# Kernel optimization log

Measured on AMD Instinct MI355X. Metric: run time of the kernel, lower is better.

Reference implementation:

```python
import jax, jax.numpy as jnp
import numpy as np

B, N, D = 4, 4096, 1024
H, DH = 16, 64  # heads, dim_head; inner_dim = H*DH = 1024
EPS = 1e-6


def setup_inputs() -> dict:
    key = jax.random.key(0)
    ks = jax.random.split(key, 6)
    s = 1.0 / np.sqrt(D)
    return {
        "x": jax.random.normal(ks[0], (B, N, D), dtype=jnp.float32),
        "Wq": jax.random.normal(ks[1], (D, H * DH), dtype=jnp.float32) * s,
        "Wk": jax.random.normal(ks[2], (D, H * DH), dtype=jnp.float32) * s,
        "Wv": jax.random.normal(ks[3], (D, H * DH), dtype=jnp.float32) * s,
        "Wo": jax.random.normal(ks[4], (H * DH, D), dtype=jnp.float32) * s,
        "bo": jnp.zeros((D,), dtype=jnp.float32),
    }


def reference(x, Wq, Wk, Wv, Wo, bo):
    # projections, split heads: b n (h d) -> b h n d
    def split_heads(t):
        b, n, _ = t.shape
        return t.reshape(b, n, H, DH).transpose(0, 2, 1, 3)

    q = split_heads(x @ Wq)
    k = split_heads(x @ Wk)  # context = x (self-attention)
    v = split_heads(x @ Wv)

    # elu feature map: elu(x) + 1
    q = jax.nn.elu(q) + 1.0
    k = jax.nn.elu(k) + 1.0

    # normalizer z[b,h,n,1] = q . sum_n k  + eps
    k_sum = k.sum(axis=2)                                  # b h d
    z = jnp.einsum('bhnd,bhd->bhn', q, k_sum)[..., None] + EPS

    # kv outer-product reduction: O(N d^2)
    kv = jnp.einsum('bhnd,bhne->bhde', k, v)               # b h d e
    out = jnp.einsum('bhnd,bhde->bhne', q, kv) / z         # b h n e

    # merge heads: b h n d -> b n (h d)
    out = out.transpose(0, 2, 1, 3).reshape(x.shape[0], x.shape[1], H * DH)
    return out @ Wo + bo
```

## Files before the change

### kernel.cpp

```cpp
#include <hip/hip_runtime.h>
#include <hip/hip_bf16.h>


#define DEV_INLINE __device__ __forceinline__

typedef short bf16x8 __attribute__((ext_vector_type(8)));
typedef float f32x4  __attribute__((ext_vector_type(4)));

static constexpr int Bb = 4, Nn = 4096, Dd = 1024, Hh = 16, DHd = 64;
static constexpr int Mrows = Bb * Nn;

DEV_INLINE float bf2f(short s) {
  unsigned u = ((unsigned)(unsigned short)s) << 16;
  float f; __builtin_memcpy(&f, &u, 4); return f;
}
DEV_INLINE short f2bf(float f) {
  unsigned u; __builtin_memcpy(&u, &f, 4);
  unsigned r = (u + 0x7fffu + ((u >> 16) & 1u)) >> 16;
  return (short)r;
}

DEV_INLINE void gload16(const void* g, void* l) {
  typedef __attribute__((address_space(1))) const void gv_t;
  typedef __attribute__((address_space(3))) void lv_t;
  __builtin_amdgcn_global_load_lds((gv_t*)g, (lv_t*)l, 16, 0, 0);
}

DEV_INLINE int lds_off(int r_, int c_) {
  return r_ * 128 + ((((c_ >> 3) ^ (r_ & 7)) << 3) | (c_ & 7));
}


__global__ void convert_x_kernel(const float* __restrict__ x, short* __restrict__ xb) {
  int i = blockIdx.x * 256 + threadIdx.x;
  float4 v = ((const float4*)x)[i];
  short4 o;
  o.x = f2bf(v.x); o.y = f2bf(v.y); o.z = f2bf(v.z); o.w = f2bf(v.w);
  ((short4*)xb)[i] = o;
}

__global__ void transposeW_kernel(const float* __restrict__ W, short* __restrict__ Wt) {
  __shared__ float tile[64][69];
  int t = threadIdx.x;
  int r = t >> 2, c4 = (t & 3) << 4;
  const float* src = W + (blockIdx.y * 64 + r) * 1024 + blockIdx.x * 64 + c4;
  for (int j = 0; j < 4; ++j) {
    float4 v = ((const float4*)src)[j];
    tile[r][c4 + 4 * j + 0] = v.x;
    tile[r][c4 + 4 * j + 1] = v.y;
    tile[r][c4 + 4 * j + 2] = v.z;
    tile[r][c4 + 4 * j + 3] = v.w;
  }
  __syncthreads();
  __attribute__((aligned(16))) short tmp[16];
  for (int j = 0; j < 16; ++j) tmp[j] = f2bf(tile[c4 + j][r]);
  short* dst = Wt + (blockIdx.x * 64 + r) * 1024 + blockIdx.y * 64 + c4;
  ((int4*)dst)[0] = ((int4*)tmp)[0];
  ((int4*)dst)[1] = ((int4*)tmp)[1];
}

template <int MODE>
__global__ __launch_bounds__(256, 2) void gemm128_kernel(
    const short* __restrict__ A, const short* __restrict__ Bt,
    short* __restrict__ q, short* __restrict__ kT, short* __restrict__ vT,
    float* __restrict__ out, const float* __restrict__ bias, int nTilesN) {
  __shared__ __align__(16) short sm[128 * 128];
  short* smA = sm;
  short* smB = sm + 8192;
  const int K = 1024;
  int bid0 = blockIdx.x;
  int xcd = bid0 & 7, local = bid0 >> 3;
  int chunk = local >> 6, rem = local & 63;
  int ncc = nTilesN >> 3;
  int cm = chunk / ncc, cn = chunk % ncc;
  int tm = xcd * 16 + cm * 8 + (rem >> 3);
  int tn = cn * 8 + (rem & 7);

  int t = threadIdx.x, w = t >> 6, lane = t & 63;
  int rl = lane & 15, kg = lane >> 4;
  int wr = w >> 1, wc = w & 1;
  const short* Abase = A + (size_t)tm * 128 * K;
  const short* Bbase = Bt + (size_t)tn * 128 * K;

  f32x4 acc[4][4] = {};
  for (int k0 = 0; k0 < K; k0 += 64) {
    __syncthreads();
    for (int p = 0; p < 4; ++p) {
      int c = p * 256 + t;
      int row = c >> 3, off = (c & 7) << 3;
      gload16(Abase + row * K + k0 + off, (char*)smA + p * 4096 + w * 1024);
      gload16(Bbase + row * K + k0 + off, (char*)smB + p * 4096 + w * 1024);
    }
    __syncthreads();
    for (int kk = 0; kk < 2; ++kk) {
      int kb = kk * 32 + kg * 8;
      bf16x8 af[4], bfr[4];
      for (int mt = 0; mt < 4; ++mt)
        af[mt] = *(const bf16x8*)&smA[(wr * 64 + mt * 16 + rl) * 64 + kb];
      for (int nt = 0; nt < 4; ++nt)
        bfr[nt] = *(const bf16x8*)&smB[(wc * 64 + nt * 16 + rl) * 64 + kb];
      for (int mt = 0; mt < 4; ++mt)
        for (int nt = 0; nt < 4; ++nt)
          acc[mt][nt] = __builtin_amdgcn_mfma_f32_16x16x32_bf16(af[mt], bfr[nt], acc[mt][nt], 0, 0, 0);
    }
  }
  if (MODE == 1) {
    for (int mt = 0; mt < 4; ++mt) {
      int grow_base = tm * 128 + wr * 64 + mt * 16 + kg * 4;
      for (int nt = 0; nt < 4; ++nt) {
        int gcol = tn * 128 + wc * 64 + nt * 16 + rl;
        float bv = bias[gcol];
        for (int r = 0; r < 4; ++r)
          out[(size_t)(grow_base + r) * Dd + gcol] = acc[mt][nt][r] + bv;
      }
    }
    return;
  }
  __syncthreads();
  int sec = tn >> 3;
  int tloc = tn & 7;
  for (int mt = 0; mt < 4; ++mt)
    for (int nt = 0; nt < 4; ++nt)
      for (int r = 0; r < 4; ++r) {
        float v = acc[mt][nt][r];
        if (sec <= 1) v = v > 0.f ? v + 1.f : __expf(v);
        int row = wr * 64 + mt * 16 + kg * 4 + r;
        int col = wc * 64 + nt * 16 + rl;
        int o = (sec == 0) ? lds_off(row, col) : lds_off(col, row);
        sm[o] = f2bf(v);
      }
  __syncthreads();
  if (sec == 0) {
    for (int i = 0; i < 8; ++i) {
      int idx = i * 256 + t;
      int row = idx >> 4, c = idx & 15;
      int col0 = c * 8;
      int gcol = tloc * 128 + col0;
      int h = gcol >> 6, d0 = gcol & 63;
      int grow = tm * 128 + row;
      int b = grow >> 12, n = grow & 4095;
      *(int4*)&q[(((size_t)(b * Hh + h)) * Nn + n) * DHd + d0] = *(const int4*)&sm[lds_off(row, col0)];
    }
  } else {
    short* dst = (sec == 1) ? kT : vT;
    for (int i = 0; i < 8; ++i) {
      int idx = i * 256 + t;
      int dcol = idx >> 4, c = idx & 15;
      int n0 = c * 8;
      int gcol = tloc * 128 + dcol;
      int h = gcol >> 6, d = gcol & 63;
      int grow0 = tm * 128 + n0;
      int b = grow0 >> 12, n = grow0 & 4095;
      *(int4*)&dst[(((size_t)(b * Hh + h)) * DHd + d) * Nn + n] = *(const int4*)&sm[lds_off(dcol, n0)];
    }
  }
}

__global__ void ksum_kernel(const short* __restrict__ kT, float* __restrict__ ksp) {
  int bh = blockIdx.x >> 3, seg = blockIdx.x & 7;
  int t = threadIdx.x;
  int d = t >> 2, sub = t & 3;
  const short* row = kT + ((size_t)bh * DHd + d) * Nn + seg * 512;
  float s = 0.f;
  for (int i = sub * 8; i < 512; i += 32) {
    bf16x8 v = *(const bf16x8*)&row[i];
    for (int j = 0; j < 8; ++j) s += bf2f(v[j]);
  }
  s += __shfl_xor(s, 1);
  s += __shfl_xor(s, 2);
  if (sub == 0) ksp[(bh * 8 + seg) * 64 + d] = s;
}

__global__ __launch_bounds__(256, 2) void kv_kernel(const short* __restrict__ kT,
                                                    const short* __restrict__ vT,
                                                    float* __restrict__ kvp) {
  __shared__ __align__(16) short smK[64 * 128];
  __shared__ __align__(16) short smV[64 * 128];
  int bh = blockIdx.x, seg = blockIdx.y;
  int t = threadIdx.x;
  int w = t >> 6, lane = t & 63, rl = lane & 15, kg = lane >> 4;
  const short* kb = kT + (size_t)bh * DHd * Nn + seg * 1024;
  const short* vb = vT + (size_t)bh * DHd * Nn + seg * 1024;
  f32x4 acc[4] = {};
  for (int n0 = 0; n0 < 1024; n0 += 128) {
    __syncthreads();
    for (int p = 0; p < 4; ++p) {
      int c = p * 256 + t;
      int row = c >> 4, off = (c & 15) << 3;
      gload16(kb + row * Nn + n0 + off, (char*)smK + p * 4096 + w * 1024);
      gload16(vb + row * Nn + n0 + off, (char*)smV + p * 4096 + w * 1024);
    }
    __syncthreads();
    for (int kk = 0; kk < 4; ++kk) {
      int kb2 = kk * 32 + kg * 8;
      bf16x8 a = *(const bf16x8*)&smK[(w * 16 + rl) * 128 + kb2];
      for (int nt = 0; nt < 4; ++nt) {
        bf16x8 b = *(const bf16x8*)&smV[(nt * 16 + rl) * 128 + kb2];
        acc[nt] = __builtin_amdgcn_mfma_f32_16x16x32_bf16(a, b, acc[nt], 0, 0, 0);
      }
    }
  }
  float* dst = kvp + ((size_t)(bh * 4 + seg)) * 4096;
  for (int nt = 0; nt < 4; ++nt)
    for (int r = 0; r < 4; ++r)
      dst[(nt * 16 + rl) * 64 + (w * 16 + kg * 4 + r)] = acc[nt][r];
}

__global__ void kvc_kernel(const float* __restrict__ kvp, short* __restrict__ kvT) {
  int bh = blockIdx.x, t = threadIdx.x;
  const float* p0 = kvp + (size_t)bh * 4 * 4096;
  for (int rep = 0; rep < 4; ++rep) {
    int idx = rep * 1024 + t * 4;
    float4 a = *(const float4*)&p0[idx];
    float4 b = *(const float4*)&p0[4096 + idx];
    float4 c = *(const float4*)&p0[8192 + idx];
    float4 d = *(const float4*)&p0[12288 + idx];
    short4 o;
    o.x = f2bf(a.x + b.x + c.x + d.x);
    o.y = f2bf(a.y + b.y + c.y + d.y);
    o.z = f2bf(a.z + b.z + c.z + d.z);
    o.w = f2bf(a.w + b.w + c.w + d.w);
    *(short4*)&kvT[(size_t)bh * 4096 + idx] = o;
  }
}

__global__ __launch_bounds__(256, 2) void attn_kernel(const short* __restrict__ q,
                                                      const short* __restrict__ kvT,
                                                      const float* __restrict__ ksp,
                                                      short* __restrict__ attn) {
  int rb = blockIdx.x, bh = blockIdx.y;
  int b = bh >> 4, h = bh & 15;
  __shared__ float sks[64];
  int t = threadIdx.x, w = t >> 6, lane = t & 63, rl = lane & 15, kg = lane >> 4;
  if (t < 64) {
    float s = 0.f;
    for (int j = 0; j < 8; ++j) s += ksp[(bh * 8 + j) * 64 + t];
    sks[t] = s;
  }
  __syncthreads();
  int row0 = rb * 64 + w * 16;
  const short* qb = q + ((size_t)bh * Nn + row0) * DHd;
  const short* kvb = kvT + (size_t)bh * 4096;
  f32x4 acc[4] = {};
  float zp = 0.f;
  for (int kk = 0; kk < 2; ++kk) {
    int kb = kk * 32 + kg * 8;
    bf16x8 a = *(const bf16x8*)&qb[rl * DHd + kb];
    for (int j = 0; j < 8; ++j) zp += bf2f(a[j]) * sks[kb + j];
    for (int nt = 0; nt < 4; ++nt) {
      bf16x8 bfr = *(const bf16x8*)&kvb[(nt * 16 + rl) * 64 + kb];
      acc[nt] = __builtin_amdgcn_mfma_f32_16x16x32_bf16(a, bfr, acc[nt], 0, 0, 0);
    }
  }
  zp += __shfl_xor(zp, 16);
  zp += __shfl_xor(zp, 32);
  float zr[4];
  for (int r = 0; r < 4; ++r) zr[r] = __shfl(zp, kg * 4 + r);
  for (int nt = 0; nt < 4; ++nt)
    for (int r = 0; r < 4; ++r) {
      int n = row0 + kg * 4 + r;
      int e = nt * 16 + rl;
      attn[((size_t)(b * Nn + n)) * 1024 + h * 64 + e] = f2bf(acc[nt][r] / (zr[r] + 1e-6f));
    }
}

extern "C" void kernel_launch(void* const* d_in, const int* in_sizes, int n_in,
                              void* d_out, int out_size, void* d_ws, size_t ws_size,
                              hipStream_t stream) {
  const float* x  = (const float*)d_in[0];
  const float* Wq = (const float*)d_in[1];
  const float* Wk = (const float*)d_in[2];
  const float* Wv = (const float*)d_in[3];
  const float* Wo = (const float*)d_in[4];
  const float* bo = (const float*)d_in[5];
  float* out = (float*)d_out;

  char* ws = (char*)d_ws;
  size_t off = 0;
  auto alloc = [&](size_t bytes) {
    char* p = ws + off;
    off += (bytes + 255) & ~(size_t)255;
    return p;
  };
  short* xb   = (short*)alloc((size_t)Mrows * 1024 * 2);
  short* Wt   = (short*)alloc((size_t)3072 * 1024 * 2);
  short* WoT  = (short*)alloc((size_t)1024 * 1024 * 2);
  short* qb   = (short*)alloc((size_t)64 * Nn * DHd * 2);
  short* kT   = (short*)alloc((size_t)64 * DHd * Nn * 2);
  short* vT   = (short*)alloc((size_t)64 * DHd * Nn * 2);
  float* ksp  = (float*)alloc((size_t)64 * 8 * 64 * 4);
  float* kvp  = (float*)alloc((size_t)64 * 4 * 4096 * 4);
  short* kvT  = (short*)alloc((size_t)64 * 4096 * 2);
  short* attn = (short*)alloc((size_t)Mrows * 1024 * 2);

  convert_x_kernel<<<16384, 256, 0, stream>>>(x, xb);
  transposeW_kernel<<<dim3(16, 16), 256, 0, stream>>>(Wq, Wt);
  transposeW_kernel<<<dim3(16, 16), 256, 0, stream>>>(Wk, Wt + 1024 * 1024);
  transposeW_kernel<<<dim3(16, 16), 256, 0, stream>>>(Wv, Wt + 2 * 1024 * 1024);
  transposeW_kernel<<<dim3(16, 16), 256, 0, stream>>>(Wo, WoT);

  gemm128_kernel<0><<<3072, 256, 0, stream>>>(xb, Wt, qb, kT, vT, nullptr, nullptr, 24);
  ksum_kernel<<<512, 256, 0, stream>>>(kT, ksp);
  kv_kernel<<<dim3(64, 4), 256, 0, stream>>>(kT, vT, kvp);
  kvc_kernel<<<64, 256, 0, stream>>>(kvp, kvT);
  attn_kernel<<<dim3(64, 64), 256, 0, stream>>>(qb, kvT, ksp, attn);
  gemm128_kernel<1><<<1024, 256, 0, stream>>>(attn, WoT, nullptr, nullptr, nullptr, out, bo, 8);
}
```

Baseline: 275.0 us.

## Swizzle LDS tiles, stage epilogue stores through LDS, merge weight transposes

Measured after the change: 239.6 us. 12.9% less time.

```diff
diff --git a/kernel.cpp b/kernel.cpp
--- a/kernel.cpp
+++ b/kernel.cpp
@@ -32,14 +32,21 @@
 
 
 __global__ void convert_x_kernel(const float* __restrict__ x, short* __restrict__ xb) {
-  int i = blockIdx.x * 256 + threadIdx.x;
-  float4 v = ((const float4*)x)[i];
-  short4 o;
-  o.x = f2bf(v.x); o.y = f2bf(v.y); o.z = f2bf(v.z); o.w = f2bf(v.w);
-  ((short4*)xb)[i] = o;
-}
-
-__global__ void transposeW_kernel(const float* __restrict__ W, short* __restrict__ Wt) {
+  const int total = Mrows * 1024 / 4;
+  for (int i = blockIdx.x * 256 + threadIdx.x; i < total; i += 2048 * 256) {
+    float4 v = ((const float4*)x)[i];
+    short4 o;
+    o.x = f2bf(v.x); o.y = f2bf(v.y); o.z = f2bf(v.z); o.w = f2bf(v.w);
+    ((short4*)xb)[i] = o;
+  }
+}
+
+__global__ void transposeW_kernel(const float* __restrict__ Wq, const float* __restrict__ Wk,
+                                  const float* __restrict__ Wv, const float* __restrict__ Wo,
+                                  short* __restrict__ Wt, short* __restrict__ WoT) {
+  int z = blockIdx.z;
+  const float* W = (z == 0) ? Wq : (z == 1) ? Wk : (z == 2) ? Wv : Wo;
+  short* dstb = (z < 3) ? (Wt + (size_t)z * 1024 * 1024) : WoT;
   __shared__ float tile[64][69];
   int t = threadIdx.x;
   int r = t >> 2, c4 = (t & 3) << 4;
@@ -54,7 +61,7 @@
   __syncthreads();
   __attribute__((aligned(16))) short tmp[16];
   for (int j = 0; j < 16; ++j) tmp[j] = f2bf(tile[c4 + j][r]);
-  short* dst = Wt + (blockIdx.x * 64 + r) * 1024 + blockIdx.y * 64 + c4;
+  short* dst = dstb + (blockIdx.x * 64 + r) * 1024 + blockIdx.y * 64 + c4;
   ((int4*)dst)[0] = ((int4*)tmp)[0];
   ((int4*)dst)[1] = ((int4*)tmp)[1];
 }
@@ -87,32 +94,48 @@
     __syncthreads();
     for (int p = 0; p < 4; ++p) {
       int c = p * 256 + t;
-      int row = c >> 3, off = (c & 7) << 3;
+      int row = c >> 3, u = c & 7;
+      int off = ((u ^ (row & 7)) << 3);
       gload16(Abase + row * K + k0 + off, (char*)smA + p * 4096 + w * 1024);
       gload16(Bbase + row * K + k0 + off, (char*)smB + p * 4096 + w * 1024);
     }
     __syncthreads();
     for (int kk = 0; kk < 2; ++kk) {
-      int kb = kk * 32 + kg * 8;
+      int slot = kk * 4 + kg;
       bf16x8 af[4], bfr[4];
-      for (int mt = 0; mt < 4; ++mt)
-        af[mt] = *(const bf16x8*)&smA[(wr * 64 + mt * 16 + rl) * 64 + kb];
-      for (int nt = 0; nt < 4; ++nt)
-        bfr[nt] = *(const bf16x8*)&smB[(wc * 64 + nt * 16 + rl) * 64 + kb];
+      for (int mt = 0; mt < 4; ++mt) {
+        int row = wr * 64 + mt * 16 + rl;
+        af[mt] = *(const bf16x8*)&smA[row * 64 + ((slot ^ (row & 7)) << 3)];
+      }
+      for (int nt = 0; nt < 4; ++nt) {
+        int row = wc * 64 + nt * 16 + rl;
+        bfr[nt] = *(const bf16x8*)&smB[row * 64 + ((slot ^ (row & 7)) << 3)];
+      }
       for (int mt = 0; mt < 4; ++mt)
         for (int nt = 0; nt < 4; ++nt)
           acc[mt][nt] = __builtin_amdgcn_mfma_f32_16x16x32_bf16(af[mt], bfr[nt], acc[mt][nt], 0, 0, 0);
     }
   }
   if (MODE == 1) {
-    for (int mt = 0; mt < 4; ++mt) {
-      int grow_base = tm * 128 + wr * 64 + mt * 16 + kg * 4;
-      for (int nt = 0; nt < 4; ++nt) {
-        int gcol = tn * 128 + wc * 64 + nt * 16 + rl;
-        float bv = bias[gcol];
-        for (int r = 0; r < 4; ++r)
-          out[(size_t)(grow_base + r) * Dd + gcol] = acc[mt][nt][r] + bv;
-      }
+    float* smf = (float*)sm;
+    __syncthreads();
+    for (int h = 0; h < 2; ++h) {
+      if (wr == h) {
+        for (int mt = 0; mt < 4; ++mt)
+          for (int nt = 0; nt < 4; ++nt)
+            for (int r = 0; r < 4; ++r)
+              smf[(mt * 16 + kg * 4 + r) * 128 + wc * 64 + nt * 16 + rl] = acc[mt][nt][r];
+      }
+      __syncthreads();
+      for (int i = 0; i < 8; ++i) {
+        int idx = i * 256 + t;
+        int row = idx >> 5, c4 = (idx & 31) << 2;
+        float4 v = *(const float4*)&smf[row * 128 + c4];
+        float4 bv = *(const float4*)&bias[tn * 128 + c4];
+        v.x += bv.x; v.y += bv.y; v.z += bv.z; v.w += bv.w;
+        *(float4*)&out[(size_t)(tm * 128 + h * 64 + row) * Dd + tn * 128 + c4] = v;
+      }
+      __syncthreads();
     }
     return;
   }
@@ -186,24 +209,35 @@
     __syncthreads();
     for (int p = 0; p < 4; ++p) {
       int c = p * 256 + t;
-      int row = c >> 4, off = (c & 15) << 3;
+      int row = c >> 4, u = c & 15;
+      int off = ((u ^ (row & 15)) << 3);
       gload16(kb + row * Nn + n0 + off, (char*)smK + p * 4096 + w * 1024);
       gload16(vb + row * Nn + n0 + off, (char*)smV + p * 4096 + w * 1024);
     }
     __syncthreads();
     for (int kk = 0; kk < 4; ++kk) {
-      int kb2 = kk * 32 + kg * 8;
-      bf16x8 a = *(const bf16x8*)&smK[(w * 16 + rl) * 128 + kb2];
+      int slot = kk * 4 + kg;
+      int rowA = w * 16 + rl;
+      bf16x8 a = *(const bf16x8*)&smK[rowA * 128 + ((slot ^ (rowA & 15)) << 3)];
       for (int nt = 0; nt < 4; ++nt) {
-        bf16x8 b = *(const bf16x8*)&smV[(nt * 16 + rl) * 128 + kb2];
+        int rowB = nt * 16 + rl;
+        bf16x8 b = *(const bf16x8*)&smV[rowB * 128 + ((slot ^ (rowB & 15)) << 3)];
         acc[nt] = __builtin_amdgcn_mfma_f32_16x16x32_bf16(a, b, acc[nt], 0, 0, 0);
       }
     }
   }
-  float* dst = kvp + ((size_t)(bh * 4 + seg)) * 4096;
+  float* smf = (float*)smK;
+  __syncthreads();
   for (int nt = 0; nt < 4; ++nt)
     for (int r = 0; r < 4; ++r)
-      dst[(nt * 16 + rl) * 64 + (w * 16 + kg * 4 + r)] = acc[nt][r];
+      smf[(nt * 16 + rl) * 64 + (w * 16 + kg * 4 + r)] = acc[nt][r];
+  __syncthreads();
+  float* dst = kvp + ((size_t)(bh * 4 + seg)) * 4096;
+  for (int i = 0; i < 4; ++i) {
+    int idx = i * 256 + t;
+    int e = idx >> 4, c4 = (idx & 15) << 2;
+    *(float4*)&dst[e * 64 + c4] = *(const float4*)&smf[e * 64 + c4];
+  }
 }
 
 __global__ void kvc_kernel(const float* __restrict__ kvp, short* __restrict__ kvT) {
@@ -231,6 +265,7 @@
   int rb = blockIdx.x, bh = blockIdx.y;
   int b = bh >> 4, h = bh & 15;
   __shared__ float sks[64];
+  __shared__ __align__(16) short satt[64 * 64];
   int t = threadIdx.x, w = t >> 6, lane = t & 63, rl = lane & 15, kg = lane >> 4;
   if (t < 64) {
     float s = 0.f;
@@ -257,11 +292,15 @@
   float zr[4];
   for (int r = 0; r < 4; ++r) zr[r] = __shfl(zp, kg * 4 + r);
   for (int nt = 0; nt < 4; ++nt)
-    for (int r = 0; r < 4; ++r) {
-      int n = row0 + kg * 4 + r;
-      int e = nt * 16 + rl;
-      attn[((size_t)(b * Nn + n)) * 1024 + h * 64 + e] = f2bf(acc[nt][r] / (zr[r] + 1e-6f));
-    }
+    for (int r = 0; r < 4; ++r)
+      satt[(w * 16 + kg * 4 + r) * 64 + nt * 16 + rl] = f2bf(acc[nt][r] / (zr[r] + 1e-6f));
+  __syncthreads();
+  for (int i = 0; i < 2; ++i) {
+    int idx = i * 256 + t;
+    int row = idx >> 3, c8 = (idx & 7) << 3;
+    int n = rb * 64 + row;
+    *(int4*)&attn[((size_t)(b * Nn + n)) * 1024 + h * 64 + c8] = *(const int4*)&satt[row * 64 + c8];
+  }
 }
 
 extern "C" void kernel_launch(void* const* d_in, const int* in_sizes, int n_in,
@@ -293,11 +332,8 @@
   short* kvT  = (short*)alloc((size_t)64 * 4096 * 2);
   short* attn = (short*)alloc((size_t)Mrows * 1024 * 2);
 
-  convert_x_kernel<<<16384, 256, 0, stream>>>(x, xb);
-  transposeW_kernel<<<dim3(16, 16), 256, 0, stream>>>(Wq, Wt);
-  transposeW_kernel<<<dim3(16, 16), 256, 0, stream>>>(Wk, Wt + 1024 * 1024);
-  transposeW_kernel<<<dim3(16, 16), 256, 0, stream>>>(Wv, Wt + 2 * 1024 * 1024);
-  transposeW_kernel<<<dim3(16, 16), 256, 0, stream>>>(Wo, WoT);
+  convert_x_kernel<<<2048, 256, 0, stream>>>(x, xb);
+  transposeW_kernel<<<dim3(16, 16, 4), 256, 0, stream>>>(Wq, Wk, Wv, Wo, Wt, WoT);
 
   gemm128_kernel<0><<<3072, 256, 0, stream>>>(xb, Wt, qb, kT, vT, nullptr, nullptr, 24);
   ksum_kernel<<<512, 256, 0, stream>>>(kT, ksp);
```
